# Kernel optimization log

Hardware: AMD Instinct MI355X
Metric: run time of the kernel (lower is better)

Reference implementation:

```python
import jax, jax.numpy as jnp
import numpy as np

B = 64          # number of trees (batch)
N = 131072      # total nodes in batch
H_ENC = 512
H_DEC = 512


def setup_inputs() -> dict:
    key = jax.random.key(0)
    k1, k2, k3, k4, k5 = jax.random.split(key, 5)
    hidden_states = jax.random.normal(k1, (B, H_DEC), dtype=jnp.float32)
    encoder_output = jax.random.normal(k2, (N, H_ENC), dtype=jnp.float32)
    # sorted segment ids encode ragged tree membership (same info as tree_sizes)
    segment_ids = jnp.sort(jax.random.randint(k3, (N,), 0, B)).astype(jnp.int32)
    # linear: nn.Linear(h_dec + h_enc, h_enc, bias=False) -> weight [h_enc, h_dec+h_enc]
    W = jax.random.normal(k4, (H_ENC, H_DEC + H_ENC), dtype=jnp.float32) / np.float32(np.sqrt(H_DEC + H_ENC))
    # v: torch.rand(h_enc, 1)
    v = jax.random.uniform(k5, (H_ENC, 1), dtype=jnp.float32)
    return {"hidden_states": hidden_states, "encoder_output": encoder_output,
            "segment_ids": segment_ids, "W": W, "v": v}


def reference(hidden_states, encoder_output, segment_ids, W, v):
    # repeat each tree's decoder state over its nodes: [N, h_dec]
    repeated = hidden_states[segment_ids]
    # concat score: tanh(Linear([h_dec ; h_enc])) @ v
    cat = jnp.concatenate([repeated, encoder_output], axis=1)      # [N, h_dec+h_enc]
    energy = jnp.tanh(cat @ W.T)                                   # [N, h_enc]
    scores = energy @ v                                            # [N, 1]
    s = scores[:, 0]
    # segment-wise (per-tree) softmax over ragged node groups
    seg_max = jax.ops.segment_max(s, segment_ids, num_segments=B)
    e = jnp.exp(s - seg_max[segment_ids])
    denom = jax.ops.segment_sum(e, segment_ids, num_segments=B)
    att = e / denom[segment_ids]
    return att[:, None]                                            # [N, 1]
```

## Files before the change

kernel.cpp:

```cpp
#include <hip/hip_runtime.h>
#include <math.h>

#define NROWS 131072
#define NSEG  64
#define HH    512
#define LDK   40

typedef unsigned short u16;
typedef unsigned int   u32;
typedef __attribute__((ext_vector_type(8))) short short8;
typedef __attribute__((ext_vector_type(8))) u16   us8;
typedef __attribute__((ext_vector_type(4))) float f32x4;

__device__ __forceinline__ u32 f2u(float f){ union {float f; u32 u;} c; c.f=f; return c.u; }
__device__ __forceinline__ float u2f(u32 u){ union {u32 u; float f;} c; c.u=u; return c.f; }
__device__ __forceinline__ u16 bf16_rne(float f){
  u32 u = f2u(f);
  u32 r = u + 0x7FFFu + ((u >> 16) & 1u);
  return (u16)(r >> 16);
}
__device__ __forceinline__ float fast_tanh(float x){
  float e = __expf(2.0f * x);
  return 1.0f - __fdividef(2.0f, e + 1.0f);
}

__global__ __launch_bounds__(256)
void hproj_kernel(const float* __restrict__ hidden, const float* __restrict__ W,
                  float* __restrict__ hproj)
{
  const int b   = blockIdx.x;
  const int tid = threadIdx.x;
  __shared__ float sh[HH];
  sh[tid]       = hidden[b * HH + tid];
  sh[tid + 256] = hidden[b * HH + tid + 256];
  __syncthreads();
  #pragma unroll
  for (int jj = 0; jj < 2; jj++) {
    const int j = jj * 256 + tid;
    const float* wrow = W + (size_t)j * 1024;
    float acc = 0.f;
    for (int k = 0; k < HH; k += 4) {
      float4 w4 = *(const float4*)(wrow + k);
      acc += sh[k] * w4.x + sh[k+1] * w4.y + sh[k+2] * w4.z + sh[k+3] * w4.w;
    }
    hproj[b * HH + j] = acc;
  }
}

__global__ __launch_bounds__(256)
void w2split_kernel(const float* __restrict__ W, u16* __restrict__ hi, u16* __restrict__ lo)
{
  const int idx = blockIdx.x * 256 + threadIdx.x;
  const int j = idx >> 9, k = idx & 511;
  const float x = W[(size_t)j * 1024 + 512 + k];
  const u32 u = f2u(x);
  hi[idx] = (u16)(u >> 16);
  lo[idx] = bf16_rne(x - u2f(u & 0xFFFF0000u));
}

__global__ __launch_bounds__(256, 3)
void gemm_score_kernel(const float* __restrict__ enc,
                       const u16* __restrict__ w2hi,
                       const u16* __restrict__ w2lo,
                       const float* __restrict__ hproj,
                       const float* __restrict__ vvec,
                       const int* __restrict__ seg,
                       float* __restrict__ scores)
{
  __shared__ u16 sAhi[128 * LDK];
  __shared__ u16 sAlo[128 * LDK];
  __shared__ u16 sBhi[128 * LDK];
  __shared__ u16 sBlo[128 * LDK];

  const int tid  = threadIdx.x;
  const int bx   = blockIdx.x;
  const int row0 = (bx >> 2) * 128;
  const int col0 = (bx & 3) * 128;

  const int wave = tid >> 6;
  const int lane = tid & 63;
  const int wr   = (wave >> 1) * 64;
  const int wc   = (wave & 1) * 64;
  const int l15  = lane & 15;
  const int quad = lane >> 4;

  const int sr = tid >> 1;
  const int sk = (tid & 1) * 16;

  f32x4 acc[4][4];
  #pragma unroll
  for (int i = 0; i < 4; i++)
    #pragma unroll
    for (int j = 0; j < 4; j++)
      acc[i][j] = (f32x4){0.f, 0.f, 0.f, 0.f};

  const float* gA  = enc  + (size_t)(row0 + sr) * HH + sk;
  const u16*   gBh = w2hi + (size_t)(col0 + sr) * HH + sk;
  const u16*   gBl = w2lo + (size_t)(col0 + sr) * HH + sk;
  u16* wAhi = &sAhi[sr * LDK + sk];
  u16* wAlo = &sAlo[sr * LDK + sk];
  u16* wBhi = &sBhi[sr * LDK + sk];
  u16* wBlo = &sBlo[sr * LDK + sk];

  for (int ks = 0; ks < HH; ks += 32) {
    float xb[16];
    *(float4*)(&xb[0])  = *(const float4*)(gA + ks + 0);
    *(float4*)(&xb[4])  = *(const float4*)(gA + ks + 4);
    *(float4*)(&xb[8])  = *(const float4*)(gA + ks + 8);
    *(float4*)(&xb[12]) = *(const float4*)(gA + ks + 12);
    u16 hb[16], lb[16];
    #pragma unroll
    for (int i = 0; i < 16; i++) {
      const u32 u = f2u(xb[i]);
      hb[i] = (u16)(u >> 16);
      lb[i] = bf16_rne(xb[i] - u2f(u & 0xFFFF0000u));
    }
    *(us8*)(wAhi)     = *(const us8*)&hb[0];
    *(us8*)(wAhi + 8) = *(const us8*)&hb[8];
    *(us8*)(wAlo)     = *(const us8*)&lb[0];
    *(us8*)(wAlo + 8) = *(const us8*)&lb[8];
    *(us8*)(wBhi)     = *(const us8*)(gBh + ks);
    *(us8*)(wBhi + 8) = *(const us8*)(gBh + ks + 8);
    *(us8*)(wBlo)     = *(const us8*)(gBl + ks);
    *(us8*)(wBlo + 8) = *(const us8*)(gBl + ks + 8);
    __syncthreads();

    short8 bhf[4], blf[4];
    #pragma unroll
    for (int j = 0; j < 4; j++) {
      const int br = (wc + j * 16 + l15) * LDK + quad * 8;
      bhf[j] = *(const short8*)&sBhi[br];
      blf[j] = *(const short8*)&sBlo[br];
    }
    #pragma unroll
    for (int i = 0; i < 4; i++) {
      const int ar = (wr + i * 16 + l15) * LDK + quad * 8;
      const short8 ah = *(const short8*)&sAhi[ar];
      const short8 al = *(const short8*)&sAlo[ar];
      #pragma unroll
      for (int j = 0; j < 4; j++) {
        acc[i][j] = __builtin_amdgcn_mfma_f32_16x16x32_bf16(ah, bhf[j], acc[i][j], 0, 0, 0);
        acc[i][j] = __builtin_amdgcn_mfma_f32_16x16x32_bf16(al, bhf[j], acc[i][j], 0, 0, 0);
        acc[i][j] = __builtin_amdgcn_mfma_f32_16x16x32_bf16(ah, blf[j], acc[i][j], 0, 0, 0);
      }
    }
    __syncthreads();
  }

  int   jn[4];
  float vv[4];
  #pragma unroll
  for (int j = 0; j < 4; j++) { jn[j] = col0 + wc + j * 16 + l15; vv[j] = vvec[jn[j]]; }

  #pragma unroll
  for (int i = 0; i < 4; i++) {
    #pragma unroll
    for (int r = 0; r < 4; r++) {
      const int gn = row0 + wr + i * 16 + quad * 4 + r;
      const float* hp = hproj + (size_t)seg[gn] * HH;
      float p = 0.f;
      #pragma unroll
      for (int j = 0; j < 4; j++) {
        const float c = acc[i][j][r] + hp[jn[j]];
        p += fast_tanh(c) * vv[j];
      }
      p += __shfl_xor(p, 1);
      p += __shfl_xor(p, 2);
      p += __shfl_xor(p, 4);
      p += __shfl_xor(p, 8);
      if (l15 == 0) atomicAdd(&scores[gn], p);
    }
  }
}

__global__ __launch_bounds__(256)
void seg_softmax_kernel(const float* __restrict__ scores, const int* __restrict__ seg,
                        float* __restrict__ out)
{
  const int b    = blockIdx.x;
  const int tid  = threadIdx.x;
  const int wv   = tid >> 6;
  const int lane = tid & 63;
  __shared__ float red[4];

  int lo = 0, hi = NROWS;
  while (lo < hi) { int mid = (lo + hi) >> 1; if (seg[mid] < b) lo = mid + 1; else hi = mid; }
  const int start = lo;
  lo = 0; hi = NROWS;
  while (lo < hi) { int mid = (lo + hi) >> 1; if (seg[mid] < b + 1) lo = mid + 1; else hi = mid; }
  const int end = lo;

  float lm = -3.4e38f;
  for (int i = start + tid; i < end; i += 256) lm = fmaxf(lm, scores[i]);
  #pragma unroll
  for (int o = 32; o; o >>= 1) lm = fmaxf(lm, __shfl_xor(lm, o));
  if (lane == 0) red[wv] = lm;
  __syncthreads();
  const float gm = fmaxf(fmaxf(red[0], red[1]), fmaxf(red[2], red[3]));
  __syncthreads();

  float ls = 0.f;
  for (int i = start + tid; i < end; i += 256) ls += expf(scores[i] - gm);
  #pragma unroll
  for (int o = 32; o; o >>= 1) ls += __shfl_xor(ls, o);
  if (lane == 0) red[wv] = ls;
  __syncthreads();
  const float denom = red[0] + red[1] + red[2] + red[3];
  const float inv = 1.0f / denom;

  for (int i = start + tid; i < end; i += 256) out[i] = expf(scores[i] - gm) * inv;
}

extern "C" void kernel_launch(void* const* d_in, const int* in_sizes, int n_in,
                              void* d_out, int out_size, void* d_ws, size_t ws_size,
                              hipStream_t stream)
{
  const float* hidden = (const float*)d_in[0];
  const float* enc    = (const float*)d_in[1];
  const int*   seg    = (const int*)d_in[2];
  const float* W      = (const float*)d_in[3];
  const float* vvec   = (const float*)d_in[4];
  float* out = (float*)d_out;

  float* scores = (float*)d_ws;
  float* hproj  = scores + NROWS;
  u16*   w2hi   = (u16*)(hproj + NSEG * HH);
  u16*   w2lo   = w2hi + (size_t)HH * HH;

  hipMemsetAsync(scores, 0, NROWS * sizeof(float), stream);
  hproj_kernel<<<NSEG, 256, 0, stream>>>(hidden, W, hproj);
  w2split_kernel<<<(HH * HH) / 256, 256, 0, stream>>>(W, w2hi, w2lo);
  gemm_score_kernel<<<(NROWS / 128) * 4, 256, 0, stream>>>(enc, w2hi, w2lo, hproj, vvec, seg, scores);
  seg_softmax_kernel<<<NSEG, 256, 0, stream>>>(scores, seg, out);
}
```

Measured before the change: 628.8 us.

## Pre-split encoder to bf16 hi/lo and stream tiles via global_load_lds

Adds a pass that converts the fp32 encoder output into bf16 hi/lo arrays in workspace once. A new GEMM kernel then loads those tiles straight into LDS with global_load_lds, instead of converting in registers on every column-block (each row was re-split four times). The hproj kernel is also rewritten to use wave-level shuffle reductions. The trade-off is an extra full pass over encoder memory (read 256MB, write 256MB) and unpadded LDS rows that may cause bank conflicts. The fallback path runs only if the workspace is too small.

```diff
diff --git a/kernel.cpp b/kernel.cpp
--- a/kernel.cpp
+++ b/kernel.cpp
@@ -23,27 +23,49 @@
   float e = __expf(2.0f * x);
   return 1.0f - __fdividef(2.0f, e + 1.0f);
 }
+__device__ __forceinline__ void gload_lds16(const void* g, void* l) {
+  __builtin_amdgcn_global_load_lds((const __attribute__((address_space(1))) void*)g,
+                                   (__attribute__((address_space(3))) void*)l, 16, 0, 0);
+}
+
+__global__ __launch_bounds__(256)
+void enc_split_kernel(const float* __restrict__ enc, u16* __restrict__ hi, u16* __restrict__ lo)
+{
+  const size_t i0 = ((size_t)blockIdx.x * 256 + threadIdx.x) * 8;
+  float4 a = *(const float4*)(enc + i0);
+  float4 b = *(const float4*)(enc + i0 + 4);
+  float x[8] = {a.x, a.y, a.z, a.w, b.x, b.y, b.z, b.w};
+  u16 h[8], l[8];
+  #pragma unroll
+  for (int i = 0; i < 8; i++) {
+    const u32 u = f2u(x[i]);
+    h[i] = (u16)(u >> 16);
+    l[i] = bf16_rne(x[i] - u2f(u & 0xFFFF0000u));
+  }
+  *(us8*)(hi + i0) = *(const us8*)h;
+  *(us8*)(lo + i0) = *(const us8*)l;
+}
 
 __global__ __launch_bounds__(256)
 void hproj_kernel(const float* __restrict__ hidden, const float* __restrict__ W,
                   float* __restrict__ hproj)
 {
-  const int b   = blockIdx.x;
-  const int tid = threadIdx.x;
-  __shared__ float sh[HH];
-  sh[tid]       = hidden[b * HH + tid];
-  sh[tid + 256] = hidden[b * HH + tid + 256];
-  __syncthreads();
-  #pragma unroll
-  for (int jj = 0; jj < 2; jj++) {
-    const int j = jj * 256 + tid;
-    const float* wrow = W + (size_t)j * 1024;
-    float acc = 0.f;
-    for (int k = 0; k < HH; k += 4) {
-      float4 w4 = *(const float4*)(wrow + k);
-      acc += sh[k] * w4.x + sh[k+1] * w4.y + sh[k+2] * w4.z + sh[k+3] * w4.w;
-    }
-    hproj[b * HH + j] = acc;
+  const int b    = blockIdx.x;
+  const int tid  = threadIdx.x;
+  const int wave = tid >> 6;
+  const int lane = tid & 63;
+  const float* hrow = hidden + (size_t)b * HH + lane * 8;
+  const float4 h0 = *(const float4*)(hrow);
+  const float4 h1 = *(const float4*)(hrow + 4);
+  for (int j = wave; j < HH; j += 4) {
+    const float* wrow = W + (size_t)j * 1024 + lane * 8;
+    const float4 w0 = *(const float4*)(wrow);
+    const float4 w1 = *(const float4*)(wrow + 4);
+    float acc = h0.x*w0.x + h0.y*w0.y + h0.z*w0.z + h0.w*w0.w
+              + h1.x*w1.x + h1.y*w1.y + h1.z*w1.z + h1.w*w1.w;
+    #pragma unroll
+    for (int o = 32; o; o >>= 1) acc += __shfl_xor(acc, o);
+    if (lane == 0) hproj[(size_t)b * HH + j] = acc;
   }
 }
 
@@ -59,18 +81,15 @@
 }
 
 __global__ __launch_bounds__(256, 3)
-void gemm_score_kernel(const float* __restrict__ enc,
-                       const u16* __restrict__ w2hi,
-                       const u16* __restrict__ w2lo,
-                       const float* __restrict__ hproj,
-                       const float* __restrict__ vvec,
-                       const int* __restrict__ seg,
-                       float* __restrict__ scores)
-{
-  __shared__ u16 sAhi[128 * LDK];
-  __shared__ u16 sAlo[128 * LDK];
-  __shared__ u16 sBhi[128 * LDK];
-  __shared__ u16 sBlo[128 * LDK];
+void gemm_fast_kernel(const u16* __restrict__ eh, const u16* __restrict__ el,
+                      const u16* __restrict__ w2hi, const u16* __restrict__ w2lo,
+                      const float* __restrict__ hproj, const float* __restrict__ vvec,
+                      const int* __restrict__ seg, float* __restrict__ scores)
+{
+  __shared__ u16 sAh[128 * 32];
+  __shared__ u16 sAl[128 * 32];
+  __shared__ u16 sBh[128 * 32];
+  __shared__ u16 sBl[128 * 32];
 
   const int tid  = threadIdx.x;
   const int bx   = blockIdx.x;
@@ -84,8 +103,14 @@
   const int l15  = lane & 15;
   const int quad = lane >> 4;
 
-  const int sr = tid >> 1;
-  const int sk = (tid & 1) * 16;
+  const int rr    = tid >> 2;
+  const int coff  = (tid & 3) * 8;
+  const int wbase = (tid >> 6) * 512;
+
+  const u16* gAh = eh   + (size_t)(row0 + rr) * HH + coff;
+  const u16* gAl = el   + (size_t)(row0 + rr) * HH + coff;
+  const u16* gBh = w2hi + (size_t)(col0 + rr) * HH + coff;
+  const u16* gBl = w2lo + (size_t)(col0 + rr) * HH + coff;
 
   f32x4 acc[4][4];
   #pragma unroll
@@ -94,49 +119,29 @@
     for (int j = 0; j < 4; j++)
       acc[i][j] = (f32x4){0.f, 0.f, 0.f, 0.f};
 
-  const float* gA  = enc  + (size_t)(row0 + sr) * HH + sk;
-  const u16*   gBh = w2hi + (size_t)(col0 + sr) * HH + sk;
-  const u16*   gBl = w2lo + (size_t)(col0 + sr) * HH + sk;
-  u16* wAhi = &sAhi[sr * LDK + sk];
-  u16* wAlo = &sAlo[sr * LDK + sk];
-  u16* wBhi = &sBhi[sr * LDK + sk];
-  u16* wBlo = &sBlo[sr * LDK + sk];
-
   for (int ks = 0; ks < HH; ks += 32) {
-    float xb[16];
-    *(float4*)(&xb[0])  = *(const float4*)(gA + ks + 0);
-    *(float4*)(&xb[4])  = *(const float4*)(gA + ks + 4);
-    *(float4*)(&xb[8])  = *(const float4*)(gA + ks + 8);
-    *(float4*)(&xb[12]) = *(const float4*)(gA + ks + 12);
-    u16 hb[16], lb[16];
-    #pragma unroll
-    for (int i = 0; i < 16; i++) {
-      const u32 u = f2u(xb[i]);
-      hb[i] = (u16)(u >> 16);
-      lb[i] = bf16_rne(xb[i] - u2f(u & 0xFFFF0000u));
-    }
-    *(us8*)(wAhi)     = *(const us8*)&hb[0];
-    *(us8*)(wAhi + 8) = *(const us8*)&hb[8];
-    *(us8*)(wAlo)     = *(const us8*)&lb[0];
-    *(us8*)(wAlo + 8) = *(const us8*)&lb[8];
-    *(us8*)(wBhi)     = *(const us8*)(gBh + ks);
-    *(us8*)(wBhi + 8) = *(const us8*)(gBh + ks + 8);
-    *(us8*)(wBlo)     = *(const us8*)(gBl + ks);
-    *(us8*)(wBlo + 8) = *(const us8*)(gBl + ks + 8);
+    gload_lds16(gAh + ks,            &sAh[wbase]);
+    gload_lds16(gAh + ks + 64 * HH,  &sAh[2048 + wbase]);
+    gload_lds16(gAl + ks,            &sAl[wbase]);
+    gload_lds16(gAl + ks + 64 * HH,  &sAl[2048 + wbase]);
+    gload_lds16(gBh + ks,            &sBh[wbase]);
+    gload_lds16(gBh + ks + 64 * HH,  &sBh[2048 + wbase]);
+    gload_lds16(gBl + ks,            &sBl[wbase]);
+    gload_lds16(gBl + ks + 64 * HH,  &sBl[2048 + wbase]);
     __syncthreads();
 
     short8 bhf[4], blf[4];
     #pragma unroll
     for (int j = 0; j < 4; j++) {
-      const int br = (wc + j * 16 + l15) * LDK + quad * 8;
-      bhf[j] = *(const short8*)&sBhi[br];
-      blf[j] = *(const short8*)&sBlo[br];
+      const int br = (wc + j * 16 + l15) * 32 + quad * 8;
+      bhf[j] = *(const short8*)&sBh[br];
+      blf[j] = *(const short8*)&sBl[br];
     }
     #pragma unroll
     for (int i = 0; i < 4; i++) {
-      const int ar = (wr + i * 16 + l15) * LDK + quad * 8;
-      const short8 ah = *(const short8*)&sAhi[ar];
-      const short8 al = *(const short8*)&sAlo[ar];
+      const int ar = (wr + i * 16 + l15) * 32 + quad * 8;
+      const short8 ah = *(const short8*)&sAh[ar];
+      const short8 al = *(const short8*)&sAl[ar];
       #pragma unroll
       for (int j = 0; j < 4; j++) {
         acc[i][j] = __builtin_amdgcn_mfma_f32_16x16x32_bf16(ah, bhf[j], acc[i][j], 0, 0, 0);
@@ -173,6 +178,121 @@
   }
 }
 
+__global__ __launch_bounds__(256, 3)
+void gemm_score_kernel(const float* __restrict__ enc,
+                       const u16* __restrict__ w2hi,
+                       const u16* __restrict__ w2lo,
+                       const float* __restrict__ hproj,
+                       const float* __restrict__ vvec,
+                       const int* __restrict__ seg,
+                       float* __restrict__ scores)
+{
+  __shared__ u16 sAhi[128 * LDK];
+  __shared__ u16 sAlo[128 * LDK];
+  __shared__ u16 sBhi[128 * LDK];
+  __shared__ u16 sBlo[128 * LDK];
+
+  const int tid  = threadIdx.x;
+  const int bx   = blockIdx.x;
+  const int row0 = (bx >> 2) * 128;
+  const int col0 = (bx & 3) * 128;
+
+  const int wave = tid >> 6;
+  const int lane = tid & 63;
+  const int wr   = (wave >> 1) * 64;
+  const int wc   = (wave & 1) * 64;
+  const int l15  = lane & 15;
+  const int quad = lane >> 4;
+
+  const int sr = tid >> 1;
+  const int sk = (tid & 1) * 16;
+
+  f32x4 acc[4][4];
+  #pragma unroll
+  for (int i = 0; i < 4; i++)
+    #pragma unroll
+    for (int j = 0; j < 4; j++)
+      acc[i][j] = (f32x4){0.f, 0.f, 0.f, 0.f};
+
+  const float* gA  = enc  + (size_t)(row0 + sr) * HH + sk;
+  const u16*   gBh = w2hi + (size_t)(col0 + sr) * HH + sk;
+  const u16*   gBl = w2lo + (size_t)(col0 + sr) * HH + sk;
+  u16* wAhi = &sAhi[sr * LDK + sk];
+  u16* wAlo = &sAlo[sr * LDK + sk];
+  u16* wBhi = &sBhi[sr * LDK + sk];
+  u16* wBlo = &sBlo[sr * LDK + sk];
+
+  for (int ks = 0; ks < HH; ks += 32) {
+    float xb[16];
+    *(float4*)(&xb[0])  = *(const float4*)(gA + ks + 0);
+    *(float4*)(&xb[4])  = *(const float4*)(gA + ks + 4);
+    *(float4*)(&xb[8])  = *(const float4*)(gA + ks + 8);
+    *(float4*)(&xb[12]) = *(const float4*)(gA + ks + 12);
+    u16 hb[16], lb[16];
+    #pragma unroll
+    for (int i = 0; i < 16; i++) {
+      const u32 u = f2u(xb[i]);
+      hb[i] = (u16)(u >> 16);
+      lb[i] = bf16_rne(xb[i] - u2f(u & 0xFFFF0000u));
+    }
+    *(us8*)(wAhi)     = *(const us8*)&hb[0];
+    *(us8*)(wAhi + 8) = *(const us8*)&hb[8];
+    *(us8*)(wAlo)     = *(const us8*)&lb[0];
+    *(us8*)(wAlo + 8) = *(const us8*)&lb[8];
+    *(us8*)(wBhi)     = *(const us8*)(gBh + ks);
+    *(us8*)(wBhi + 8) = *(const us8*)(gBh + ks + 8);
+    *(us8*)(wBlo)     = *(const us8*)(gBl + ks);
+    *(us8*)(wBlo + 8) = *(const us8*)(gBl + ks + 8);
+    __syncthreads();
+
+    short8 bhf[4], blf[4];
+    #pragma unroll
+    for (int j = 0; j < 4; j++) {
+      const int br = (wc + j * 16 + l15) * LDK + quad * 8;
+      bhf[j] = *(const short8*)&sBhi[br];
+      blf[j] = *(const short8*)&sBlo[br];
+    }
+    #pragma unroll
+    for (int i = 0; i < 4; i++) {
+      const int ar = (wr + i * 16 + l15) * LDK + quad * 8;
+      const short8 ah = *(const short8*)&sAhi[ar];
+      const short8 al = *(const short8*)&sAlo[ar];
+      #pragma unroll
+      for (int j = 0; j < 4; j++) {
+        acc[i][j] = __builtin_amdgcn_mfma_f32_16x16x32_bf16(ah, bhf[j], acc[i][j], 0, 0, 0);
+        acc[i][j] = __builtin_amdgcn_mfma_f32_16x16x32_bf16(al, bhf[j], acc[i][j], 0, 0, 0);
+        acc[i][j] = __builtin_amdgcn_mfma_f32_16x16x32_bf16(ah, blf[j], acc[i][j], 0, 0, 0);
+      }
+    }
+    __syncthreads();
+  }
+
+  int   jn[4];
+  float vv[4];
+  #pragma unroll
+  for (int j = 0; j < 4; j++) { jn[j] = col0 + wc + j * 16 + l15; vv[j] = vvec[jn[j]]; }
+
+  #pragma unroll
+  for (int i = 0; i < 4; i++) {
+    #pragma unroll
+    for (int r = 0; r < 4; r++) {
+      const int gn = row0 + wr + i * 16 + quad * 4 + r;
+      const float* hp = hproj + (size_t)seg[gn] * HH;
+      float p = 0.f;
+      #pragma unroll
+      for (int j = 0; j < 4; j++) {
+        const float c = acc[i][j][r] + hp[jn[j]];
+        p += fast_tanh(c) * vv[j];
+      }
+      p += __shfl_xor(p, 1);
+      p += __shfl_xor(p, 2);
+      p += __shfl_xor(p, 4);
+      p += __shfl_xor(p, 8);
+      if (l15 == 0) atomicAdd(&scores[gn], p);
+    }
+  }
+}
+
 __global__ __launch_bounds__(256)
 void seg_softmax_kernel(const float* __restrict__ scores, const int* __restrict__ seg,
                         float* __restrict__ out)
@@ -226,10 +346,23 @@
   float* hproj  = scores + NROWS;
   u16*   w2hi   = (u16*)(hproj + NSEG * HH);
   u16*   w2lo   = w2hi + (size_t)HH * HH;
+  u16*   encHi  = w2lo + (size_t)HH * HH;
+  u16*   encLo  = encHi + (size_t)NROWS * HH;
+
+  const size_t need_big = (size_t)NROWS * 4 + (size_t)NSEG * HH * 4
+                        + (size_t)HH * HH * 2 * 2 + (size_t)NROWS * HH * 2 * 2;
 
   hipMemsetAsync(scores, 0, NROWS * sizeof(float), stream);
   hproj_kernel<<<NSEG, 256, 0, stream>>>(hidden, W, hproj);
   w2split_kernel<<<(HH * HH) / 256, 256, 0, stream>>>(W, w2hi, w2lo);
-  gemm_score_kernel<<<(NROWS / 128) * 4, 256, 0, stream>>>(enc, w2hi, w2lo, hproj, vvec, seg, scores);
+
+  if (ws_size >= need_big) {
+    enc_split_kernel<<<(NROWS * HH) / (256 * 8), 256, 0, stream>>>(enc, encHi, encLo);
+    gemm_fast_kernel<<<(NROWS / 128) * 4, 256, 0, stream>>>(encHi, encLo, w2hi, w2lo,
+                                                            hproj, vvec, seg, scores);
+  } else {
+    gemm_score_kernel<<<(NROWS / 128) * 4, 256, 0, stream>>>(enc, w2hi, w2lo,
+                                                             hproj, vvec, seg, scores);
+  }
   seg_softmax_kernel<<<NSEG, 256, 0, stream>>>(scores, seg, out);
 }
```

Measured after the change: 738.8 us. 1.17x slower.

## Stream fp32 A tiles via global_load_lds with XOR swizzle; split bf16 at fragment load

Applied to the files above, without the earlier changes.

The GEMM now stages the fp32 encoder tile and the bf16 weight tiles directly into LDS with global_load_lds, using XOR-swizzled layouts instead of padded rows. The hi/lo bf16 split of A moves from the staging phase to after the LDS fragment read. This removes register round-trips and staging stores, but redoes the split for every column wave and doubles the LDS footprint for A. The low part is now truncated rather than rounded to nearest even, and hproj is reworked to use a wave-per-row dot product with shuffle reduction.

```diff
diff --git a/kernel.cpp b/kernel.cpp
--- a/kernel.cpp
+++ b/kernel.cpp
@@ -4,13 +4,13 @@
 #define NROWS 131072
 #define NSEG  64
 #define HH    512
-#define LDK   40
 
 typedef unsigned short u16;
 typedef unsigned int   u32;
 typedef __attribute__((ext_vector_type(8))) short short8;
 typedef __attribute__((ext_vector_type(8))) u16   us8;
 typedef __attribute__((ext_vector_type(4))) float f32x4;
+typedef __attribute__((ext_vector_type(4))) u32   u32x4;
 
 __device__ __forceinline__ u32 f2u(float f){ union {float f; u32 u;} c; c.f=f; return c.u; }
 __device__ __forceinline__ float u2f(u32 u){ union {u32 u; float f;} c; c.u=u; return c.f; }
@@ -23,27 +23,31 @@
   float e = __expf(2.0f * x);
   return 1.0f - __fdividef(2.0f, e + 1.0f);
 }
+__device__ __forceinline__ void gload_lds16(const void* g, void* l) {
+  __builtin_amdgcn_global_load_lds((const __attribute__((address_space(1))) void*)g,
+                                   (__attribute__((address_space(3))) void*)l, 16, 0, 0);
+}
 
 __global__ __launch_bounds__(256)
 void hproj_kernel(const float* __restrict__ hidden, const float* __restrict__ W,
                   float* __restrict__ hproj)
 {
-  const int b   = blockIdx.x;
-  const int tid = threadIdx.x;
-  __shared__ float sh[HH];
-  sh[tid]       = hidden[b * HH + tid];
-  sh[tid + 256] = hidden[b * HH + tid + 256];
-  __syncthreads();
-  #pragma unroll
-  for (int jj = 0; jj < 2; jj++) {
-    const int j = jj * 256 + tid;
-    const float* wrow = W + (size_t)j * 1024;
-    float acc = 0.f;
-    for (int k = 0; k < HH; k += 4) {
-      float4 w4 = *(const float4*)(wrow + k);
-      acc += sh[k] * w4.x + sh[k+1] * w4.y + sh[k+2] * w4.z + sh[k+3] * w4.w;
-    }
-    hproj[b * HH + j] = acc;
+  const int b    = blockIdx.x;
+  const int tid  = threadIdx.x;
+  const int wave = tid >> 6;
+  const int lane = tid & 63;
+  const float* hrow = hidden + (size_t)b * HH + lane * 8;
+  const float4 h0 = *(const float4*)(hrow);
+  const float4 h1 = *(const float4*)(hrow + 4);
+  for (int j = wave; j < HH; j += 4) {
+    const float* wrow = W + (size_t)j * 1024 + lane * 8;
+    const float4 w0 = *(const float4*)(wrow);
+    const float4 w1 = *(const float4*)(wrow + 4);
+    float acc = h0.x*w0.x + h0.y*w0.y + h0.z*w0.z + h0.w*w0.w
+              + h1.x*w1.x + h1.y*w1.y + h1.z*w1.z + h1.w*w1.w;
+    #pragma unroll
+    for (int o = 32; o; o >>= 1) acc += __shfl_xor(acc, o);
+    if (lane == 0) hproj[(size_t)b * HH + j] = acc;
   }
 }
 
@@ -59,18 +63,14 @@
 }
 
 __global__ __launch_bounds__(256, 3)
-void gemm_score_kernel(const float* __restrict__ enc,
-                       const u16* __restrict__ w2hi,
-                       const u16* __restrict__ w2lo,
-                       const float* __restrict__ hproj,
-                       const float* __restrict__ vvec,
-                       const int* __restrict__ seg,
-                       float* __restrict__ scores)
-{
-  __shared__ u16 sAhi[128 * LDK];
-  __shared__ u16 sAlo[128 * LDK];
-  __shared__ u16 sBhi[128 * LDK];
-  __shared__ u16 sBlo[128 * LDK];
+void gemm_fused_kernel(const float* __restrict__ enc,
+                       const u16* __restrict__ w2hi, const u16* __restrict__ w2lo,
+                       const float* __restrict__ hproj, const float* __restrict__ vvec,
+                       const int* __restrict__ seg, float* __restrict__ scores)
+{
+  __shared__ float sAf[128 * 32];
+  __shared__ u16   sBh[128 * 32];
+  __shared__ u16   sBl[128 * 32];
 
   const int tid  = threadIdx.x;
   const int bx   = blockIdx.x;
@@ -84,8 +84,16 @@
   const int l15  = lane & 15;
   const int quad = lane >> 4;
 
-  const int sr = tid >> 1;
-  const int sk = (tid & 1) * 16;
+  const int arow = tid >> 3;
+  const int acol = ((tid & 7) ^ (arow & 6)) * 4;
+  const float* gA = enc + (size_t)(row0 + arow) * HH + acol;
+  const int awb = (tid >> 6) * 256;
+
+  const int brow = tid >> 2;
+  const int bcol = ((tid & 3) ^ ((brow >> 1) & 3)) * 8;
+  const u16* gBh = w2hi + (size_t)(col0 + brow) * HH + bcol;
+  const u16* gBl = w2lo + (size_t)(col0 + brow) * HH + bcol;
+  const int bwb = (tid >> 6) * 512;
 
   f32x4 acc[4][4];
   #pragma unroll
@@ -94,54 +102,47 @@
     for (int j = 0; j < 4; j++)
       acc[i][j] = (f32x4){0.f, 0.f, 0.f, 0.f};
 
-  const float* gA  = enc  + (size_t)(row0 + sr) * HH + sk;
-  const u16*   gBh = w2hi + (size_t)(col0 + sr) * HH + sk;
-  const u16*   gBl = w2lo + (size_t)(col0 + sr) * HH + sk;
-  u16* wAhi = &sAhi[sr * LDK + sk];
-  u16* wAlo = &sAlo[sr * LDK + sk];
-  u16* wBhi = &sBhi[sr * LDK + sk];
-  u16* wBlo = &sBlo[sr * LDK + sk];
-
   for (int ks = 0; ks < HH; ks += 32) {
-    float xb[16];
-    *(float4*)(&xb[0])  = *(const float4*)(gA + ks + 0);
-    *(float4*)(&xb[4])  = *(const float4*)(gA + ks + 4);
-    *(float4*)(&xb[8])  = *(const float4*)(gA + ks + 8);
-    *(float4*)(&xb[12]) = *(const float4*)(gA + ks + 12);
-    u16 hb[16], lb[16];
-    #pragma unroll
-    for (int i = 0; i < 16; i++) {
-      const u32 u = f2u(xb[i]);
-      hb[i] = (u16)(u >> 16);
-      lb[i] = bf16_rne(xb[i] - u2f(u & 0xFFFF0000u));
+    #pragma unroll
+    for (int i = 0; i < 4; i++)
+      gload_lds16(gA + (size_t)i * 32 * HH + ks, &sAf[i * 1024 + awb]);
+    gload_lds16(gBh + ks,                      &sBh[bwb]);
+    gload_lds16(gBh + (size_t)64 * HH + ks,    &sBh[2048 + bwb]);
+    gload_lds16(gBl + ks,                      &sBl[bwb]);
+    gload_lds16(gBl + (size_t)64 * HH + ks,    &sBl[2048 + bwb]);
+    __syncthreads();
+
+    short8 bhf[4], blf[4];
+    #pragma unroll
+    for (int j = 0; j < 4; j++) {
+      const int r  = wc + j * 16 + l15;
+      const int off = r * 32 + 8 * (quad ^ ((r >> 1) & 3));
+      bhf[j] = *(const short8*)&sBh[off];
+      blf[j] = *(const short8*)&sBl[off];
     }
-    *(us8*)(wAhi)     = *(const us8*)&hb[0];
-    *(us8*)(wAhi + 8) = *(const us8*)&hb[8];
-    *(us8*)(wAlo)     = *(const us8*)&lb[0];
-    *(us8*)(wAlo + 8) = *(const us8*)&lb[8];
-    *(us8*)(wBhi)     = *(const us8*)(gBh + ks);
-    *(us8*)(wBhi + 8) = *(const us8*)(gBh + ks + 8);
-    *(us8*)(wBlo)     = *(const us8*)(gBl + ks);
-    *(us8*)(wBlo + 8) = *(const us8*)(gBl + ks + 8);
-    __syncthreads();
-
-    short8 bhf[4], blf[4];
-    #pragma unroll
-    for (int j = 0; j < 4; j++) {
-      const int br = (wc + j * 16 + l15) * LDK + quad * 8;
-      bhf[j] = *(const short8*)&sBhi[br];
-      blf[j] = *(const short8*)&sBlo[br];
-    }
+
     #pragma unroll
     for (int i = 0; i < 4; i++) {
-      const int ar = (wr + i * 16 + l15) * LDK + quad * 8;
-      const short8 ah = *(const short8*)&sAhi[ar];
-      const short8 al = *(const short8*)&sAlo[ar];
+      const int r  = wr + i * 16 + l15;
+      const int ab = r * 32 + 8 * (quad ^ ((r >> 1) & 3));
+      const f32x4 x0 = *(const f32x4*)&sAf[ab];
+      const f32x4 x1 = *(const f32x4*)&sAf[ab + 4];
+      union { u32x4 w; short8 s; } ah, al;
+      #pragma unroll
+      for (int p = 0; p < 4; p++) {
+        const float xa = (p < 2) ? x0[2 * p] : x1[2 * p - 4];
+        const float xb = (p < 2) ? x0[2 * p + 1] : x1[2 * p - 3];
+        const u32 ua = f2u(xa), ub = f2u(xb);
+        ah.w[p] = (ua >> 16) | (ub & 0xFFFF0000u);
+        const float ra = xa - u2f(ua & 0xFFFF0000u);
+        const float rb = xb - u2f(ub & 0xFFFF0000u);
+        al.w[p] = (f2u(ra) >> 16) | (f2u(rb) & 0xFFFF0000u);
+      }
       #pragma unroll
       for (int j = 0; j < 4; j++) {
-        acc[i][j] = __builtin_amdgcn_mfma_f32_16x16x32_bf16(ah, bhf[j], acc[i][j], 0, 0, 0);
-        acc[i][j] = __builtin_amdgcn_mfma_f32_16x16x32_bf16(al, bhf[j], acc[i][j], 0, 0, 0);
-        acc[i][j] = __builtin_amdgcn_mfma_f32_16x16x32_bf16(ah, blf[j], acc[i][j], 0, 0, 0);
+        acc[i][j] = __builtin_amdgcn_mfma_f32_16x16x32_bf16(ah.s, bhf[j], acc[i][j], 0, 0, 0);
+        acc[i][j] = __builtin_amdgcn_mfma_f32_16x16x32_bf16(al.s, bhf[j], acc[i][j], 0, 0, 0);
+        acc[i][j] = __builtin_amdgcn_mfma_f32_16x16x32_bf16(ah.s, blf[j], acc[i][j], 0, 0, 0);
       }
     }
     __syncthreads();
@@ -230,6 +231,7 @@
   hipMemsetAsync(scores, 0, NROWS * sizeof(float), stream);
   hproj_kernel<<<NSEG, 256, 0, stream>>>(hidden, W, hproj);
   w2split_kernel<<<(HH * HH) / 256, 256, 0, stream>>>(W, w2hi, w2lo);
-  gemm_score_kernel<<<(NROWS / 128) * 4, 256, 0, stream>>>(enc, w2hi, w2lo, hproj, vvec, seg, scores);
+  gemm_fused_kernel<<<(NROWS / 128) * 4, 256, 0, stream>>>(enc, w2hi, w2lo,
+                                                           hproj, vvec, seg, scores);
   seg_softmax_kernel<<<NSEG, 256, 0, stream>>>(scores, seg, out);
 }
```

Result: slower. 646.1 us (+2.7%).
